# Optimization experiments

Measured on AMD Instinct MI355X. Metric: run time of the kernel, lower is better.

Reference implementation:

```python
import jax, jax.numpy as jnp
import numpy as np

B, S = 4, 4096
VOCAB = 32000
HIDDEN = 2048
INT_DIM = 64
N_LC = 8192


def _gelu(x):
    # torch nn.GELU() default is the exact (erf) formulation
    return jax.nn.gelu(x, approximate=False)


def setup_inputs() -> dict:
    key = jax.random.key(0)
    ks = jax.random.split(key, 12)
    inp = {
        "input_ids": jax.random.randint(ks[0], (B, S), 0, VOCAB, dtype=jnp.int64) if jax.config.jax_enable_x64 else jax.random.randint(ks[0], (B, S), 0, VOCAB, dtype=jnp.int32),
        "lc_values": jax.random.normal(ks[1], (N_LC, 1), dtype=jnp.float32),
        "pos_b": jax.random.randint(ks[2], (N_LC,), 0, B, dtype=jnp.int32),
        "pos_s": jax.random.randint(ks[3], (N_LC,), 0, S, dtype=jnp.int32),
        # learned params
        "wte": jax.random.normal(ks[4], (VOCAB, HIDDEN), dtype=jnp.float32) * 0.02,
        "W0": jax.random.normal(ks[5], (1, INT_DIM), dtype=jnp.float32) * 0.5,
        "b0": jnp.zeros((INT_DIM,), dtype=jnp.float32),
        "W1": jax.random.normal(ks[6], (INT_DIM, INT_DIM), dtype=jnp.float32) * (1.0 / np.sqrt(INT_DIM)),
        "b1": jnp.zeros((INT_DIM,), dtype=jnp.float32),
        "W2": jax.random.normal(ks[7], (INT_DIM, INT_DIM), dtype=jnp.float32) * (1.0 / np.sqrt(INT_DIM)),
        "b2": jnp.zeros((INT_DIM,), dtype=jnp.float32),
        "Wout": jax.random.normal(ks[8], (INT_DIM, HIDDEN), dtype=jnp.float32) * (1.0 / np.sqrt(INT_DIM)),
        "bout": jnp.zeros((HIDDEN,), dtype=jnp.float32),
    }
    return inp


def reference(input_ids, lc_values, pos_b, pos_s, wte, W0, b0, W1, b1, W2, b2, Wout, bout):
    V = wte.shape[0]
    # clamp_min(0).clamp_max(vocab_size); clip to V-1 so the gather is in-range
    ids = jnp.clip(input_ids, 0, V - 1)
    hidden = wte[ids]  # [B, S, H] embedding gather
    h = lc_values @ W0 + b0
    h = _gelu(h) @ W1 + b1
    h = _gelu(h) @ W2 + b2
    lc_features = _gelu(h) @ Wout + bout  # [N_lc, H]
    # index_put(..., accumulate=False): overwrite rows at (pos_b, pos_s)
    return hidden.at[pos_b, pos_s].set(lc_features.astype(hidden.dtype))
```

## Files before the change

kernel.cpp:

```cpp
#include <hip/hip_runtime.h>
#include <hip/hip_bf16.h>
#include <math.h>

#define BB 4
#define SS 4096
#define HH 2048
#define VOCAB 32000
#define NLC 8192
#define ROWS (BB*SS)

#define FROWS 32
#define FCOLS 512
#define FEAT_BLOCKS ((NLC / FROWS) * (HH / FCOLS))

typedef float fvec4 __attribute__((ext_vector_type(4)));

__device__ __forceinline__ float gelu_exact(float x) {
    return 0.5f * x * (1.0f + erff(x * 0.70710678118654752f));
}

__global__ void mlp_scatter_kernel(const float* __restrict__ lc, const float* __restrict__ W0,
                                   const float* __restrict__ b0, const float* __restrict__ W1,
                                   const float* __restrict__ b1, const float* __restrict__ W2,
                                   const float* __restrict__ b2, float* __restrict__ g2out,
                                   const int* __restrict__ pos_b, const int* __restrict__ pos_s,
                                   int* __restrict__ win) {
    int t = threadIdx.x;
    if (blockIdx.x < NLC / 256) {
        int i = blockIdx.x * 256 + t;
        int p = pos_b[i] * SS + pos_s[i];
        atomicMax(&win[p], i + 1);
    }

    int w = t >> 6;
    int j = t & 63;
    int row = blockIdx.x * 4 + w;
    __shared__ float g[4][64];
    float x = lc[row];
    float h = gelu_exact(fmaf(x, W0[j], b0[j]));
    g[w][j] = h;
    __syncthreads();
    float acc = b1[j];
#pragma unroll
    for (int k = 0; k < 64; ++k) acc = fmaf(g[w][k], W1[k * 64 + j], acc);
    acc = gelu_exact(acc);
    __syncthreads();
    g[w][j] = acc;
    __syncthreads();
    float acc2 = b2[j];
#pragma unroll
    for (int k = 0; k < 64; ++k) acc2 = fmaf(g[w][k], W2[k * 64 + j], acc2);
    g2out[row * 64 + j] = gelu_exact(acc2);
}

__global__ void feat_gather_kernel(const float* __restrict__ g2, const int* __restrict__ win,
                                   const int* __restrict__ pos_b, const int* __restrict__ pos_s,
                                   const float* __restrict__ Wout, const float* __restrict__ bout,
                                   const int* __restrict__ ids, const float* __restrict__ wte,
                                   float* __restrict__ out) {
    __shared__ float g2s[FROWS][64];
    __shared__ int   wrow[FROWS];
    int t = threadIdx.x;

    if (blockIdx.x < ROWS) {
        int row = blockIdx.x;
        if (win[row] > 0) return;
        int id = ids[row];
        id = id < 0 ? 0 : (id > VOCAB - 1 ? VOCAB - 1 : id);
        const fvec4* src = (const fvec4*)(wte + (size_t)id * HH);
        fvec4* dst = (fvec4*)(out + (size_t)row * HH);
        fvec4 v0 = __builtin_nontemporal_load(&src[t]);
        fvec4 v1 = __builtin_nontemporal_load(&src[t + 256]);
        __builtin_nontemporal_store(v0, &dst[t]);
        __builtin_nontemporal_store(v1, &dst[t + 256]);
        return;
    }

    int fid  = blockIdx.x - ROWS;
    int rblk = fid & 255;
    int cb   = (fid >> 8) * FCOLS;
    int base = rblk * FROWS;

    {
        const float4* src = (const float4*)(g2 + base * 64);
        float4* dst = (float4*)&g2s[0][0];
        dst[t] = src[t];
        dst[t + 256] = src[t + 256];
    }
    if (t < FROWS) {
        int i = base + t;
        int p = pos_b[i] * SS + pos_s[i];
        wrow[t] = (win[p] == i + 1) ? p : -1;
    }
    __syncthreads();

    int w = t >> 6, l = t & 63;
    const float* wbase = Wout + cb + l * 4;

    float4 bv0 = *(const float4*)&bout[cb + l * 4];
    float4 bv1 = *(const float4*)&bout[cb + 256 + l * 4];
    float4 acc0[8], acc1[8];
#pragma unroll
    for (int r = 0; r < 8; ++r) { acc0[r] = bv0; acc1[r] = bv1; }

    for (int k0 = 0; k0 < 64; k0 += 4) {
        float4 wv0[4], wv1[4];
#pragma unroll
        for (int kk = 0; kk < 4; ++kk) {
            const float* wp = wbase + (size_t)(k0 + kk) * HH;
            wv0[kk] = *(const float4*)wp;
            wv1[kk] = *(const float4*)(wp + 256);
        }
#pragma unroll
        for (int r = 0; r < 8; ++r) {
            float4 gv = *(const float4*)&g2s[w * 8 + r][k0];
#pragma unroll
            for (int c = 0; c < 4; ++c) {
                float g0 = (&gv.x)[0], g1 = (&gv.x)[1], g2v = (&gv.x)[2], g3 = (&gv.x)[3];
                (&acc0[r].x)[c] = fmaf(g0, (&wv0[0].x)[c],
                                  fmaf(g1, (&wv0[1].x)[c],
                                  fmaf(g2v, (&wv0[2].x)[c],
                                  fmaf(g3, (&wv0[3].x)[c], (&acc0[r].x)[c]))));
                (&acc1[r].x)[c] = fmaf(g0, (&wv1[0].x)[c],
                                  fmaf(g1, (&wv1[1].x)[c],
                                  fmaf(g2v, (&wv1[2].x)[c],
                                  fmaf(g3, (&wv1[3].x)[c], (&acc1[r].x)[c]))));
            }
        }
    }

#pragma unroll
    for (int r = 0; r < 8; ++r) {
        int p = wrow[w * 8 + r];
        if (p < 0) continue;
        float* op = out + (size_t)p * HH + cb + l * 4;
        *(float4*)op = acc0[r];
        *(float4*)(op + 256) = acc1[r];
    }
}

extern "C" void kernel_launch(void* const* d_in, const int* in_sizes, int n_in,
                              void* d_out, int out_size, void* d_ws, size_t ws_size,
                              hipStream_t stream) {
    const int*   ids  = (const int*)d_in[0];
    const float* lc   = (const float*)d_in[1];
    const int*   pb   = (const int*)d_in[2];
    const int*   ps   = (const int*)d_in[3];
    const float* wte  = (const float*)d_in[4];
    const float* W0   = (const float*)d_in[5];
    const float* b0   = (const float*)d_in[6];
    const float* W1   = (const float*)d_in[7];
    const float* b1   = (const float*)d_in[8];
    const float* W2   = (const float*)d_in[9];
    const float* b2   = (const float*)d_in[10];
    const float* Wout = (const float*)d_in[11];
    const float* bout = (const float*)d_in[12];
    float* out = (float*)d_out;

    int*   win = (int*)d_ws;
    float* g2  = (float*)((char*)d_ws + ROWS * sizeof(int));

    (void)hipMemsetAsync(win, 0, ROWS * sizeof(int), stream);
    mlp_scatter_kernel<<<NLC / 4, 256, 0, stream>>>(lc, W0, b0, W1, b1, W2, b2, g2, pb, ps, win);
    feat_gather_kernel<<<ROWS + FEAT_BLOCKS, 256, 0, stream>>>(g2, win, pb, ps, Wout, bout, ids, wte, out);
}
```

Before: 405.9 us.

## Fuse MLP layers into feature output kernel and split winner computation

```diff
diff --git a/kernel.cpp b/kernel.cpp
--- a/kernel.cpp
+++ b/kernel.cpp
@@ -1,5 +1,4 @@
 #include <hip/hip_runtime.h>
-#include <hip/hip_bf16.h>
 #include <math.h>
 
 #define BB 4
@@ -19,51 +18,29 @@
     return 0.5f * x * (1.0f + erff(x * 0.70710678118654752f));
 }
 
-__global__ void mlp_scatter_kernel(const float* __restrict__ lc, const float* __restrict__ W0,
-                                   const float* __restrict__ b0, const float* __restrict__ W1,
-                                   const float* __restrict__ b1, const float* __restrict__ W2,
-                                   const float* __restrict__ b2, float* __restrict__ g2out,
-                                   const int* __restrict__ pos_b, const int* __restrict__ pos_s,
-                                   int* __restrict__ win) {
-    int t = threadIdx.x;
-    if (blockIdx.x < NLC / 256) {
-        int i = blockIdx.x * 256 + t;
-        int p = pos_b[i] * SS + pos_s[i];
-        atomicMax(&win[p], i + 1);
-    }
-
-    int w = t >> 6;
-    int j = t & 63;
-    int row = blockIdx.x * 4 + w;
-    __shared__ float g[4][64];
-    float x = lc[row];
-    float h = gelu_exact(fmaf(x, W0[j], b0[j]));
-    g[w][j] = h;
-    __syncthreads();
-    float acc = b1[j];
-#pragma unroll
-    for (int k = 0; k < 64; ++k) acc = fmaf(g[w][k], W1[k * 64 + j], acc);
-    acc = gelu_exact(acc);
-    __syncthreads();
-    g[w][j] = acc;
-    __syncthreads();
-    float acc2 = b2[j];
-#pragma unroll
-    for (int k = 0; k < 64; ++k) acc2 = fmaf(g[w][k], W2[k * 64 + j], acc2);
-    g2out[row * 64 + j] = gelu_exact(acc2);
+__global__ void win_kernel(const int* __restrict__ pos_b, const int* __restrict__ pos_s,
+                           int* __restrict__ win) {
+    int i = blockIdx.x * 256 + threadIdx.x;
+    int p = pos_b[i] * SS + pos_s[i];
+    atomicMax(&win[p], i + 1);
 }
 
-__global__ void feat_gather_kernel(const float* __restrict__ g2, const int* __restrict__ win,
-                                   const int* __restrict__ pos_b, const int* __restrict__ pos_s,
-                                   const float* __restrict__ Wout, const float* __restrict__ bout,
-                                   const int* __restrict__ ids, const float* __restrict__ wte,
-                                   float* __restrict__ out) {
-    __shared__ float g2s[FROWS][64];
+__global__ void fused_kernel(const float* __restrict__ lc,
+                             const float* __restrict__ W0, const float* __restrict__ b0,
+                             const float* __restrict__ W1, const float* __restrict__ b1,
+                             const float* __restrict__ W2, const float* __restrict__ b2,
+                             const float* __restrict__ Wout, const float* __restrict__ bout,
+                             const int* __restrict__ win,
+                             const int* __restrict__ pos_b, const int* __restrict__ pos_s,
+                             const int* __restrict__ ids, const float* __restrict__ wte,
+                             float* __restrict__ out) {
+    __shared__ float bufA[FROWS][64];
+    __shared__ float bufB[FROWS][64];
     __shared__ int   wrow[FROWS];
     int t = threadIdx.x;
 
-    if (blockIdx.x < ROWS) {
-        int row = blockIdx.x;
+    if (blockIdx.x >= FEAT_BLOCKS) {
+        int row = blockIdx.x - FEAT_BLOCKS;
         if (win[row] > 0) return;
         int id = ids[row];
         id = id < 0 ? 0 : (id > VOCAB - 1 ? VOCAB - 1 : id);
@@ -76,29 +53,75 @@
         return;
     }
 
-    int fid  = blockIdx.x - ROWS;
+    int fid  = blockIdx.x;
     int rblk = fid & 255;
     int cb   = (fid >> 8) * FCOLS;
     int base = rblk * FROWS;
+    int w = t >> 6, j = t & 63;
 
-    {
-        const float4* src = (const float4*)(g2 + base * 64);
-        float4* dst = (float4*)&g2s[0][0];
-        dst[t] = src[t];
-        dst[t + 256] = src[t + 256];
-    }
     if (t < FROWS) {
         int i = base + t;
         int p = pos_b[i] * SS + pos_s[i];
         wrow[t] = (win[p] == i + 1) ? p : -1;
     }
+
+    {
+        float w0j = W0[j], b0j = b0[j];
+#pragma unroll
+        for (int r = 0; r < 8; ++r) {
+            int ri = w * 8 + r;
+            float x = lc[base + ri];
+            bufA[ri][j] = gelu_exact(fmaf(x, w0j, b0j));
+        }
+    }
+    __syncthreads();
+    {
+        float b1j = b1[j];
+        float acc[8];
+#pragma unroll
+        for (int r = 0; r < 8; ++r) acc[r] = b1j;
+#pragma unroll 4
+        for (int k0 = 0; k0 < 64; k0 += 4) {
+            float wa = W1[(k0 + 0) * 64 + j];
+            float wb = W1[(k0 + 1) * 64 + j];
+            float wc = W1[(k0 + 2) * 64 + j];
+            float wd = W1[(k0 + 3) * 64 + j];
+#pragma unroll
+            for (int r = 0; r < 8; ++r) {
+                float4 hv = *(const float4*)&bufA[w * 8 + r][k0];
+                acc[r] = fmaf(hv.x, wa, fmaf(hv.y, wb, fmaf(hv.z, wc, fmaf(hv.w, wd, acc[r]))));
+            }
+        }
+#pragma unroll
+        for (int r = 0; r < 8; ++r) bufB[w * 8 + r][j] = gelu_exact(acc[r]);
+    }
+    __syncthreads();
+    {
+        float b2j = b2[j];
+        float acc[8];
+#pragma unroll
+        for (int r = 0; r < 8; ++r) acc[r] = b2j;
+#pragma unroll 4
+        for (int k0 = 0; k0 < 64; k0 += 4) {
+            float wa = W2[(k0 + 0) * 64 + j];
+            float wb = W2[(k0 + 1) * 64 + j];
+            float wc = W2[(k0 + 2) * 64 + j];
+            float wd = W2[(k0 + 3) * 64 + j];
+#pragma unroll
+            for (int r = 0; r < 8; ++r) {
+                float4 hv = *(const float4*)&bufB[w * 8 + r][k0];
+                acc[r] = fmaf(hv.x, wa, fmaf(hv.y, wb, fmaf(hv.z, wc, fmaf(hv.w, wd, acc[r]))));
+            }
+        }
+#pragma unroll
+        for (int r = 0; r < 8; ++r) bufA[w * 8 + r][j] = gelu_exact(acc[r]);
+    }
     __syncthreads();
 
-    int w = t >> 6, l = t & 63;
-    const float* wbase = Wout + cb + l * 4;
+    const float* wbase = Wout + cb + j * 4;
 
-    float4 bv0 = *(const float4*)&bout[cb + l * 4];
-    float4 bv1 = *(const float4*)&bout[cb + 256 + l * 4];
+    float4 bv0 = *(const float4*)&bout[cb + j * 4];
+    float4 bv1 = *(const float4*)&bout[cb + 256 + j * 4];
     float4 acc0[8], acc1[8];
 #pragma unroll
     for (int r = 0; r < 8; ++r) { acc0[r] = bv0; acc1[r] = bv1; }
@@ -113,7 +136,7 @@
         }
 #pragma unroll
         for (int r = 0; r < 8; ++r) {
-            float4 gv = *(const float4*)&g2s[w * 8 + r][k0];
+            float4 gv = *(const float4*)&bufA[w * 8 + r][k0];
 #pragma unroll
             for (int c = 0; c < 4; ++c) {
                 float g0 = (&gv.x)[0], g1 = (&gv.x)[1], g2v = (&gv.x)[2], g3 = (&gv.x)[3];
@@ -133,7 +156,7 @@
     for (int r = 0; r < 8; ++r) {
         int p = wrow[w * 8 + r];
         if (p < 0) continue;
-        float* op = out + (size_t)p * HH + cb + l * 4;
+        float* op = out + (size_t)p * HH + cb + j * 4;
         *(float4*)op = acc0[r];
         *(float4*)(op + 256) = acc1[r];
     }
@@ -157,10 +180,10 @@
     const float* bout = (const float*)d_in[12];
     float* out = (float*)d_out;
 
-    int*   win = (int*)d_ws;
-    float* g2  = (float*)((char*)d_ws + ROWS * sizeof(int));
+    int* win = (int*)d_ws;
 
     (void)hipMemsetAsync(win, 0, ROWS * sizeof(int), stream);
-    mlp_scatter_kernel<<<NLC / 4, 256, 0, stream>>>(lc, W0, b0, W1, b1, W2, b2, g2, pb, ps, win);
-    feat_gather_kernel<<<ROWS + FEAT_BLOCKS, 256, 0, stream>>>(g2, win, pb, ps, Wout, bout, ids, wte, out);
+    win_kernel<<<NLC / 256, 256, 0, stream>>>(pb, ps, win);
+    fused_kernel<<<FEAT_BLOCKS + ROWS, 256, 0, stream>>>(lc, W0, b0, W1, b1, W2, b2,
+                                                         Wout, bout, win, pb, ps, ids, wte, out);
 }
```

Result: no change. 412.6 us (+1.6%).
